# Optimization experiments

Measured on AMD Instinct MI355X. Metric: run time of the kernel, lower is better.

## Reference

```python
import jax, jax.numpy as jnp
import numpy as np

TEMPERATURE = 0.07
EPS = 1e-8  # torch CosineSimilarity eps


def setup_inputs() -> dict:
    key = jax.random.key(0)
    features = jax.random.normal(key, (16, 1024, 512), dtype=jnp.float32)
    return {"features": features}


def reference(features):
    """Vectorized equivalent of the original double Python loop.

    For each b and each t in [1, T-2]:
      anchor = f[b,t], positive = f[b,t+1]
      negatives = all frames j with j < t-1 or j >= t+2  (excludes t-1, t, t+1)
      loss_bt = -log( exp(cos(a,p)/T) / (exp(cos(a,p)/T) + sum_j exp(cos(a,n_j)/T)) )
    Returns mean over all (b, t) pairs (neg pool is non-empty for all t when T > 3).
    """
    B, T, D = features.shape
    norm = jnp.maximum(jnp.linalg.norm(features, axis=-1, keepdims=True), EPS)
    n = features / norm  # [B, T, D]
    # full pairwise cosine-sim logits, scaled by temperature
    sim = jnp.einsum('btd,bsd->bts', n, n) / TEMPERATURE  # [B, T, T]

    t_idx = jnp.arange(1, T - 1)            # anchors t = 1 .. T-2
    j_idx = jnp.arange(T)
    # negatives: j in [0, t-1) union [t+2, T)  -> excludes t-1, t, t+1
    neg_mask = (j_idx[None, :] < t_idx[:, None] - 1) | (j_idx[None, :] >= t_idx[:, None] + 2)  # [T-2, T]

    logits = sim[:, 1:T - 1, :]                                   # [B, T-2, T]
    pos = logits[:, jnp.arange(T - 2), jnp.arange(2, T)]          # sim[b, t, t+1] -> [B, T-2]
    neg_logits = jnp.where(neg_mask[None], logits, -jnp.inf)
    lse_neg = jax.nn.logsumexp(neg_logits, axis=-1)               # log sum_j exp(neg_sim)
    # -log(exp(pos)/(exp(pos)+negsum)) = logaddexp(pos, lse_neg) - pos
    loss_bt = jnp.logaddexp(pos, lse_neg) - pos                   # [B, T-2]
    return jnp.mean(loss_bt)
```

## Files before the change

kernel.cpp:

```cpp
#include <hip/hip_runtime.h>
#include <hip/hip_bf16.h>
#include <hip/hip_fp8.h>

#define B_ 16
#define T_ 1024
#define D_ 512
#define EPS_ 1e-8f
#define SCALE2 20.609929155566063f
#define LN2_ 0.6931471805599453f

#define BM 128
#define BN 128
#define NKIT 4
#define SCL 0x7B7B7B7B

typedef __attribute__((ext_vector_type(4))) int   int4v;
typedef __attribute__((ext_vector_type(8))) int   int8v;
typedef __attribute__((ext_vector_type(4))) float floatx4;

typedef __attribute__((address_space(1))) const unsigned int g_u32;
typedef __attribute__((address_space(3))) unsigned int l_u32;

__device__ __forceinline__ void glds16(const void* g, void* l) {
    __builtin_amdgcn_global_load_lds((g_u32*)g, (l_u32*)l, 16, 0, 0);
}

__device__ __forceinline__ unsigned char f2e4m3(float x) {
    __hip_fp8_e4m3 q(x);
    return (unsigned char)q.__x;
}

__global__ __launch_bounds__(256) void norm_kernel(const float* __restrict__ f,
                                                   unsigned char* __restrict__ nrm,
                                                   float* __restrict__ rs_g,
                                                   float* __restrict__ rp_g,
                                                   float* __restrict__ out) {
    const int gi = blockIdx.x * 256 + threadIdx.x;
    if (gi < B_ * T_) { rs_g[gi] = 0.0f; rp_g[gi] = 0.0f; }
    if (gi == 0) out[0] = 0.0f;

    const int row  = blockIdx.x * 4 + (threadIdx.x >> 6);
    const int lane = threadIdx.x & 63;
    const size_t off = (size_t)row * D_ + lane * 8;
    const float4 v0 = *(const float4*)(f + off);
    const float4 v1 = *(const float4*)(f + off + 4);
    float ss = v0.x*v0.x + v0.y*v0.y + v0.z*v0.z + v0.w*v0.w
             + v1.x*v1.x + v1.y*v1.y + v1.z*v1.z + v1.w*v1.w;
    #pragma unroll
    for (int o = 32; o >= 1; o >>= 1) ss += __shfl_xor(ss, o, 64);
    const float sc = 16.0f / fmaxf(sqrtf(ss), EPS_);
    unsigned int w0 =  (unsigned int)f2e4m3(v0.x*sc)
                    | ((unsigned int)f2e4m3(v0.y*sc) << 8)
                    | ((unsigned int)f2e4m3(v0.z*sc) << 16)
                    | ((unsigned int)f2e4m3(v0.w*sc) << 24);
    unsigned int w1 =  (unsigned int)f2e4m3(v1.x*sc)
                    | ((unsigned int)f2e4m3(v1.y*sc) << 8)
                    | ((unsigned int)f2e4m3(v1.z*sc) << 16)
                    | ((unsigned int)f2e4m3(v1.w*sc) << 24);
    uint2 w; w.x = w0; w.y = w1;
    *(uint2*)(nrm + (size_t)row * D_ + lane * 8) = w;
}

__global__ __launch_bounds__(256, 2) void loss_kernel(const unsigned char* __restrict__ nrm,
                                                      float* __restrict__ rs_g,
                                                      float* __restrict__ rp_g) {
    const int b  = blockIdx.y;
    const int t0 = blockIdx.x * BM;
    const int j0 = blockIdx.z * BN;
    const char* base = (const char*)(nrm + (size_t)b * T_ * D_);

    __shared__ __align__(16) char Al[2][16384];
    __shared__ __align__(16) char Bl[2][16384];

    const int tid = threadIdx.x;
    const int w   = tid >> 6;
    const int l   = tid & 63;

    const int r8l = l >> 3;
    const int gch = (l & 7) ^ ((l >> 4) & 3);
    const char* sA[4];
    const char* sB[4];
    #pragma unroll
    for (int i = 0; i < 4; ++i) {
        sA[i] = base + (size_t)(t0 + w * 32 + i * 8 + r8l) * 512 + gch * 16;
        sB[i] = base + (size_t)(j0 + w * 32 + i * 8 + r8l) * 512 + gch * 16;
    }

#define ISSUE(P, KIT) do {                                                \
    _Pragma("unroll")                                                     \
    for (int i_ = 0; i_ < 4; ++i_) {                                      \
        glds16(sA[i_] + (KIT) * 128, (char*)Al[P] + w * 4096 + i_ * 1024);\
        glds16(sB[i_] + (KIT) * 128, (char*)Bl[P] + w * 4096 + i_ * 1024);\
    }                                                                     \
} while (0)

    const int wr = w >> 1, wc = w & 1;
    const int m  = l & 15;
    const int kq = l >> 4;
    const int p0 = (2 * kq) ^ ((m >> 1) & 3);
    const int rd0 = m * 128 + p0 * 16;
    const int rd1 = m * 128 + (p0 ^ 1) * 16;

    floatx4 acc[4][4] = {};

    ISSUE(0, 0);

    #pragma unroll
    for (int kit = 0; kit < NKIT; ++kit) {
        __syncthreads();
        if (kit + 1 < NKIT) ISSUE((kit + 1) & 1, kit + 1);

        const char* As = (const char*)Al[kit & 1] + wr * 8192;
        const char* Bs = (const char*)Bl[kit & 1] + wc * 8192;
        int8v af[4], bf[4];
        #pragma unroll
        for (int mi = 0; mi < 4; ++mi) {
            int4v lo = *(const int4v*)(As + mi * 2048 + rd0);
            int4v hi = *(const int4v*)(As + mi * 2048 + rd1);
            af[mi] = __builtin_shufflevector(lo, hi, 0, 1, 2, 3, 4, 5, 6, 7);
        }
        #pragma unroll
        for (int ni = 0; ni < 4; ++ni) {
            int4v lo = *(const int4v*)(Bs + ni * 2048 + rd0);
            int4v hi = *(const int4v*)(Bs + ni * 2048 + rd1);
            bf[ni] = __builtin_shufflevector(lo, hi, 0, 1, 2, 3, 4, 5, 6, 7);
        }

        #pragma unroll
        for (int mi = 0; mi < 4; ++mi)
            #pragma unroll
            for (int ni = 0; ni < 4; ++ni)
                acc[mi][ni] = __builtin_amdgcn_mfma_scale_f32_16x16x128_f8f6f4(
                    af[mi], bf[ni], acc[mi][ni],
                    0, 0,
                    0, SCL, 0, SCL);
    }
#undef ISSUE

    const int lrow = l >> 4;
    const int lcol = l & 15;
    const int bT   = b * T_;

    #pragma unroll
    for (int mi = 0; mi < 4; ++mi) {
        #pragma unroll
        for (int rg = 0; rg < 4; ++rg) {
            const int t = t0 + wr * 64 + mi * 16 + lrow * 4 + rg;
            float rsum = 0.f, rp = 0.f;
            #pragma unroll
            for (int ni = 0; ni < 4; ++ni) {
                const int j  = j0 + wc * 64 + ni * 16 + lcol;
                const float s2 = acc[mi][ni][rg] * SCALE2;
                const float e  = exp2f(s2);
                if (j < t - 1 || j > t + 1) rsum += e;
                if (j == t + 1)             rp   = s2;
            }
            #pragma unroll
            for (int o = 8; o >= 1; o >>= 1) {
                rsum += __shfl_xor(rsum, o, 64);
                rp   += __shfl_xor(rp,   o, 64);
            }
            if (lcol == 0) {
                atomicAdd(&rs_g[bT + t], rsum);
                if (rp != 0.0f) atomicAdd(&rp_g[bT + t], rp);
            }
        }
    }
}

__global__ __launch_bounds__(256) void fin_kernel(const float* __restrict__ rs_g,
                                                  const float* __restrict__ rp_g,
                                                  float* __restrict__ out) {
    const int idx = blockIdx.x * 256 + threadIdx.x;
    float v = 0.0f;
    if (idx < B_ * T_) {
        const int t = idx & (T_ - 1);
        if (t >= 1 && t <= T_ - 2) {
            const float p2 = rp_g[idx];
            const float s  = rs_g[idx];
            v = (log2f(exp2f(p2) + s) - p2) * LN2_;
        }
    }
    #pragma unroll
    for (int o = 32; o >= 1; o >>= 1) v += __shfl_xor(v, o, 64);
    __shared__ float ws_[4];
    if ((threadIdx.x & 63) == 0) ws_[threadIdx.x >> 6] = v;
    __syncthreads();
    if (threadIdx.x == 0) {
        const float scale = 1.0f / (float)(B_ * (T_ - 2));
        atomicAdd(out, (ws_[0] + ws_[1] + ws_[2] + ws_[3]) * scale);
    }
}

extern "C" void kernel_launch(void* const* d_in, const int* in_sizes, int n_in,
                              void* d_out, int out_size, void* d_ws, size_t ws_size,
                              hipStream_t stream) {
    const float* feat = (const float*)d_in[0];
    float* out = (float*)d_out;

    unsigned char* nrm = (unsigned char*)d_ws;
    float* rs_g = (float*)((char*)d_ws + (size_t)B_ * T_ * D_);
    float* rp_g = rs_g + B_ * T_;

    norm_kernel<<<B_ * T_ / 4, 256, 0, stream>>>(feat, nrm, rs_g, rp_g, out);
    loss_kernel<<<dim3(T_ / BM, B_, T_ / BN), 256, 0, stream>>>(nrm, rs_g, rp_g);
    fin_kernel<<<(B_ * T_ + 255) / 256, 256, 0, stream>>>(rs_g, rp_g, out);
}
```

Before: 105.3 us.

## Exploit similarity symmetry by computing only upper-triangular tiles with column-sum scatter

The loss kernel now launches only the upper-triangular pairs of 128x128 tiles per batch, decoding each block index into a (bi, bj) pair. Off-diagonal tiles scatter their masked exponent sums both to the rows and, through a column reduction, to the columns, so the mirrored tile is never computed. Diagonal tiles load a single operand tile and reuse it for both MFMA inputs. The aim is to cut the matmul and exp work by roughly half, in exchange for more atomics, a branchy index decode, and a grid of 576 blocks whose per-block cost is uneven and which only slightly exceeds one full wave.

```diff
diff --git a/kernel.cpp b/kernel.cpp
--- a/kernel.cpp
+++ b/kernel.cpp
@@ -10,7 +10,8 @@
 #define LN2_ 0.6931471805599453f
 
 #define BM 128
-#define BN 128
+#define NBLK 8
+#define NPAIR (NBLK * (NBLK + 1) / 2)
 #define NKIT 4
 #define SCL 0x7B7B7B7B
 
@@ -64,9 +65,15 @@
 __global__ __launch_bounds__(256, 2) void loss_kernel(const unsigned char* __restrict__ nrm,
                                                       float* __restrict__ rs_g,
                                                       float* __restrict__ rp_g) {
+    int u = blockIdx.x, bi = 0, rem = NBLK;
+    while (u >= rem) { u -= rem; --rem; ++bi; }
+    const int bj   = bi + u;
+    const bool diag = (bi == bj);
+    const bool near = (bj - bi) <= 1;
+
     const int b  = blockIdx.y;
-    const int t0 = blockIdx.x * BM;
-    const int j0 = blockIdx.z * BN;
+    const int t0 = bi * BM;
+    const int j0 = bj * BM;
     const char* base = (const char*)(nrm + (size_t)b * T_ * D_);
 
     __shared__ __align__(16) char Al[2][16384];
@@ -86,12 +93,15 @@
         sB[i] = base + (size_t)(j0 + w * 32 + i * 8 + r8l) * 512 + gch * 16;
     }
 
-#define ISSUE(P, KIT) do {                                                \
-    _Pragma("unroll")                                                     \
-    for (int i_ = 0; i_ < 4; ++i_) {                                      \
-        glds16(sA[i_] + (KIT) * 128, (char*)Al[P] + w * 4096 + i_ * 1024);\
-        glds16(sB[i_] + (KIT) * 128, (char*)Bl[P] + w * 4096 + i_ * 1024);\
-    }                                                                     \
+#define ISSUE(P, KIT) do {                                                    \
+    _Pragma("unroll")                                                         \
+    for (int i_ = 0; i_ < 4; ++i_)                                            \
+        glds16(sA[i_] + (KIT) * 128, (char*)Al[P] + w * 4096 + i_ * 1024);    \
+    if (!diag) {                                                              \
+        _Pragma("unroll")                                                     \
+        for (int i_ = 0; i_ < 4; ++i_)                                        \
+            glds16(sB[i_] + (KIT) * 128, (char*)Bl[P] + w * 4096 + i_ * 1024);\
+    }                                                                         \
 } while (0)
 
     const int wr = w >> 1, wc = w & 1;
@@ -111,7 +121,8 @@
         if (kit + 1 < NKIT) ISSUE((kit + 1) & 1, kit + 1);
 
         const char* As = (const char*)Al[kit & 1] + wr * 8192;
-        const char* Bs = (const char*)Bl[kit & 1] + wc * 8192;
+        const char* Bs = (diag ? (const char*)Al[kit & 1]
+                               : (const char*)Bl[kit & 1]) + wc * 8192;
         int8v af[4], bf[4];
         #pragma unroll
         for (int mi = 0; mi < 4; ++mi) {
@@ -140,6 +151,7 @@
     const int lrow = l >> 4;
     const int lcol = l & 15;
     const int bT   = b * T_;
+    float cs[4] = {0.f, 0.f, 0.f, 0.f};
 
     #pragma unroll
     for (int mi = 0; mi < 4; ++mi) {
@@ -152,18 +164,29 @@
                 const int j  = j0 + wc * 64 + ni * 16 + lcol;
                 const float s2 = acc[mi][ni][rg] * SCALE2;
                 const float e  = exp2f(s2);
-                if (j < t - 1 || j > t + 1) rsum += e;
-                if (j == t + 1)             rp   = s2;
+                if (j < t - 1 || j > t + 1) { rsum += e; cs[ni] += e; }
+                if (near && j == t + 1)     rp = s2;
             }
             #pragma unroll
-            for (int o = 8; o >= 1; o >>= 1) {
-                rsum += __shfl_xor(rsum, o, 64);
-                rp   += __shfl_xor(rp,   o, 64);
+            for (int o = 8; o >= 1; o >>= 1) rsum += __shfl_xor(rsum, o, 64);
+            if (near) {
+                #pragma unroll
+                for (int o = 8; o >= 1; o >>= 1) rp += __shfl_xor(rp, o, 64);
             }
             if (lcol == 0) {
                 atomicAdd(&rs_g[bT + t], rsum);
-                if (rp != 0.0f) atomicAdd(&rp_g[bT + t], rp);
+                if (near) atomicAdd(&rp_g[bT + t], rp);
             }
+        }
+    }
+    if (!diag) {
+        #pragma unroll
+        for (int ni = 0; ni < 4; ++ni) {
+            float c = cs[ni];
+            c += __shfl_xor(c, 16, 64);
+            c += __shfl_xor(c, 32, 64);
+            if (lrow == 0)
+                atomicAdd(&rs_g[bT + j0 + wc * 64 + ni * 16 + lcol], c);
         }
     }
 }
@@ -203,6 +226,6 @@
     float* rp_g = rs_g + B_ * T_;
 
     norm_kernel<<<B_ * T_ / 4, 256, 0, stream>>>(feat, nrm, rs_g, rp_g, out);
-    loss_kernel<<<dim3(T_ / BM, B_, T_ / BN), 256, 0, stream>>>(nrm, rs_g, rp_g);
+    loss_kernel<<<dim3(NPAIR, B_), 256, 0, stream>>>(nrm, rs_g, rp_g);
     fin_kernel<<<(B_ * T_ + 255) / 256, 256, 0, stream>>>(rs_g, rp_g, out);
 }
```

Result: slower. 108.4 us (+3.0%).
